# Kernel optimization log

Hardware: AMD Instinct MI355X
Metric: run time of the kernel (lower is better)

Reference implementation:

```python
import jax, jax.numpy as jnp
import numpy as np

BATCH, NUM_FEAT, EMB = 1024, 32, 16
HIDDEN = [128, 128, 128]


def setup_inputs() -> dict:
    key = jax.random.key(0)
    ks = jax.random.split(key, 4)
    inputs = jax.random.normal(ks[0], (BATCH, NUM_FEAT, EMB), dtype=jnp.float32)
    # Conv1D kernel_size=1 -> dense weight of shape (in_dim, units) per layer.
    # in_dim_i = h_{i-1} * num_feat, with h_{-1} = num_feat.
    in0 = NUM_FEAT * NUM_FEAT          # 1024
    in1 = HIDDEN[0] * NUM_FEAT         # 4096
    in2 = HIDDEN[1] * NUM_FEAT         # 4096
    scale = lambda fan_in: (1.0 / np.sqrt(fan_in)).astype(np.float32) if isinstance(fan_in, np.ndarray) else np.float32(1.0 / np.sqrt(fan_in))
    W0 = jax.random.normal(ks[1], (in0, HIDDEN[0]), dtype=jnp.float32) * scale(in0)
    W1 = jax.random.normal(ks[2], (in1, HIDDEN[1]), dtype=jnp.float32) * scale(in1)
    W2 = jax.random.normal(ks[3], (in2, HIDDEN[2]), dtype=jnp.float32) * scale(in2)
    b0 = jnp.zeros((HIDDEN[0],), dtype=jnp.float32)
    b1 = jnp.zeros((HIDDEN[1],), dtype=jnp.float32)
    b2 = jnp.zeros((HIDDEN[2],), dtype=jnp.float32)
    return {"inputs": inputs, "W0": W0, "b0": b0, "W1": W1, "b1": b1, "W2": W2, "b2": b2}


def reference(inputs, W0, b0, W1, b1, W2, b2):
    # inputs: (b, m, e) -> x0: (b, e, m)  [channels-last like tf.transpose perm=[0,2,1]]
    x0 = jnp.transpose(inputs, (0, 2, 1))
    b, d, m = x0.shape
    params = [(W0, b0), (W1, b1), (W2, b2)]
    xl = x0
    layer_outs = []
    for i, (W, bias) in enumerate(params):
        h = xl.shape[-1]
        # outer product over feature axes: (b, d, h, m) -> flatten to (b, d, h*m)
        zl = jnp.einsum('bdh,bdm->bdhm', xl, x0).reshape(b, d, h * m)
        xl = zl @ W + bias  # 1x1 conv == per-position GEMM
        if i < len(params) - 1:
            xl = jax.nn.relu(xl)
        layer_outs.append(xl)
    # sum over embedding axis d, concat over layers -> (b, sum(HIDDEN))
    return jnp.concatenate([o.sum(axis=1) for o in layer_outs], axis=1)
```

## Files before the change

### kernel.cpp

```cpp
#include <hip/hip_runtime.h>


typedef unsigned int u32;
typedef __attribute__((ext_vector_type(8))) short short8;
typedef __attribute__((ext_vector_type(4))) float f32x4;
typedef __attribute__((ext_vector_type(4))) u32 u32x4;

#define R_TOTAL 16384
#define GLOBAL_AS __attribute__((address_space(1)))
#define LDS_AS __attribute__((address_space(3)))

union PackU { u32 u[4]; short8 s; };
union PackB { u32x4 v; short8 s; };

__device__ __forceinline__ u32 pack_rne(float a, float b) {
  u32 r;
  asm("v_cvt_pk_bf16_f32 %0, %1, %2" : "=v"(r) : "v"(a), "v"(b));
  return r;
}

__device__ __forceinline__ void build_x0t_body(const float* __restrict__ in,
                                               float* __restrict__ x0t,
                                               int bid, int tid, float* t) {
  const int b0 = bid * 8;
  #pragma unroll
  for (int rep = 0; rep < 4; ++rep) {
    int idx = tid + rep * 256;
    *(float4*)&t[idx * 4] = *(const float4*)&in[(size_t)b0 * 512 + idx * 4];
  }
  __syncthreads();
  #pragma unroll
  for (int rep = 0; rep < 4; ++rep) {
    int idx = tid + rep * 256;
    int m = idx >> 5, rem = idx & 31;
    int bl = rem >> 2, dq = rem & 3;
    *(float4*)&x0t[(size_t)m * R_TOTAL + (b0 + bl) * 16 + dq * 4] =
        *(const float4*)&t[bl * 512 + m * 16 + dq * 4];
  }
}

__device__ __forceinline__ void swizzle_body(const float* __restrict__ W,
                                             u32* __restrict__ wt,
                                             int bid, int tid, float* wl) {
  const int t = bid >> 2, nq = bid & 3;
  {
    int kk = tid >> 3, c4 = tid & 7;
    float4 v = *(const float4*)&W[(size_t)(t * 32 + kk) * 128 + nq * 32 + c4 * 4];
    wl[kk * 33 + c4 * 4 + 0] = v.x;
    wl[kk * 33 + c4 * 4 + 1] = v.y;
    wl[kk * 33 + c4 * 4 + 2] = v.z;
    wl[kk * 33 + c4 * 4 + 3] = v.w;
  }
  __syncthreads();
  if (tid < 128) {
    int nl = tid >> 2, p = tid & 3;
    int q = p ^ (nl & 3);
    u32 o[4];
    #pragma unroll
    for (int jj = 0; jj < 4; ++jj)
      o[jj] = pack_rne(wl[(q * 8 + 2 * jj + 0) * 33 + nl],
                       wl[(q * 8 + 2 * jj + 1) * 33 + nl]);
    *(u32x4*)(wt + (size_t)(t * 4 + nq) * 512 + nl * 16 + p * 4) =
        u32x4{o[0], o[1], o[2], o[3]};
  }
}

__global__ __launch_bounds__(256) void prep_all(
    const float* __restrict__ in, float* __restrict__ x0t,
    const float* __restrict__ W0, u32* __restrict__ wt0,
    const float* __restrict__ W1, u32* __restrict__ wt1,
    const float* __restrict__ W2, u32* __restrict__ wt2) {
  __shared__ float sh[4096];
  const int b = blockIdx.x, tid = threadIdx.x;
  if (b < 128)      build_x0t_body(in, x0t, b, tid, sh);
  else if (b < 256) swizzle_body(W0, wt0, b - 128, tid, sh);
  else if (b < 768) swizzle_body(W1, wt1, b - 256, tid, sh);
  else              swizzle_body(W2, wt2, b - 768, tid, sh);
}

__device__ __forceinline__ void stage2k(const u32* g, u32* l, int lane) {
  const GLOBAL_AS u32* gp = (const GLOBAL_AS u32*)g;
  LDS_AS u32* lp = (LDS_AS u32*)l;
  #pragma unroll
  for (int i = 0; i < 2; ++i)
    __builtin_amdgcn_global_load_lds(gp + i * 256 + lane * 4, lp + i * 256, 16, 0, 0);
}

#define KITER(I, SLOT, WAITIMM, DO_STAGE)                                      \
  {                                                                            \
    __builtin_amdgcn_s_waitcnt(WAITIMM);                                       \
    __builtin_amdgcn_sched_barrier(0);                                         \
    f32x4 xlc[4];                                                              \
    xlc[0] = xn[SLOT][0]; xlc[1] = xn[SLOT][1];                                \
    xlc[2] = xn[SLOT][2]; xlc[3] = xn[SLOT][3];                                \
    const u32* buf = mybuf + (SLOT) * 512;                                     \
    PackB bh0, bh1;                                                            \
    {                                                                          \
      const u32* row0 = buf + ln15 * 16;                                       \
      bh0.v = *(const u32x4*)(row0 + ((q ^ sw) * 4));                          \
      const u32* row1 = buf + (16 + ln15) * 16;                                \
      bh1.v = *(const u32x4*)(row1 + ((q ^ sw) * 4));                          \
    }                                                                          \
    asm volatile("s_waitcnt lgkmcnt(0)" ::: "memory");                         \
    __builtin_amdgcn_sched_barrier(0);                                         \
    if (DO_STAGE) {                                                            \
      stage2k(wt + (size_t)((t0 + (I) + 2) * 4 + nq) * 512,                    \
              mybuf + (SLOT) * 512, lane);                                     \
      const float* xp = xt + (size_t)(t0 + (I) + 2) * R_TOTAL + r0;            \
      xn[SLOT][0] = *(const f32x4*)(xp + 0 + q * 4);                           \
      xn[SLOT][1] = *(const f32x4*)(xp + 16 + q * 4);                          \
      xn[SLOT][2] = *(const f32x4*)(xp + 32 + q * 4);                          \
      xn[SLOT][3] = *(const f32x4*)(xp + 48 + q * 4);                          \
    }                                                                          \
    __builtin_amdgcn_sched_barrier(0);                                         \
    __builtin_amdgcn_s_setprio(1);                                             \
    _Pragma("unroll")                                                          \
    for (int f = 0; f < 4; ++f) {                                              \
      f32x4 Y = __builtin_amdgcn_mfma_f32_16x16x32_bf16(Ah[f].s, bh0.s, zero4, 0, 0, 0); \
      acc[f][0] += xlc[f] * Y;                                                 \
    }                                                                          \
    _Pragma("unroll")                                                          \
    for (int f = 0; f < 4; ++f) {                                              \
      f32x4 Y = __builtin_amdgcn_mfma_f32_16x16x32_bf16(Ah[f].s, bh1.s, zero4, 0, 0, 0); \
      acc[f][1] += xlc[f] * Y;                                                 \
    }                                                                          \
    __builtin_amdgcn_s_setprio(0);                                             \
    __builtin_amdgcn_sched_barrier(0);                                         \
  }

template <int NT, bool RELU, bool STORE_X>
__global__ __launch_bounds__(512, 2) void layer_mfma(
    const float* __restrict__ xt,
    const float* __restrict__ x0t,
    const u32* __restrict__ wt,
    const float* __restrict__ bias,
    float* __restrict__ xoutT,
    float* __restrict__ osum)
{
  constexpr int HT = NT / 2;
  static_assert((HT & 1) == 0 && HT >= 4, "pair-loop needs even HT >= 4");
  __shared__ u32 smem[16384];

  const int tid = threadIdx.x;
  const int w = tid >> 6, lane = tid & 63;
  const int ln15 = lane & 15, q = lane >> 4;
  const int kh = w & 1, nq = w >> 1;
  const int r0 = blockIdx.x * 64;
  const int sw = ln15 & 3;
  u32* mybuf = smem + w * 2048;

  PackU Ah[4];
  #pragma unroll
  for (int f = 0; f < 4; ++f) {
    const int rbase = r0 + f * 16 + ln15;
    float e[8];
    #pragma unroll
    for (int j = 0; j < 8; ++j) e[j] = x0t[(size_t)(q * 8 + j) * R_TOTAL + rbase];
    #pragma unroll
    for (int jj = 0; jj < 4; ++jj)
      Ah[f].u[jj] = pack_rne(e[2 * jj], e[2 * jj + 1]);
  }

  f32x4 acc[4][2];
  #pragma unroll
  for (int f = 0; f < 4; ++f)
    #pragma unroll
    for (int c = 0; c < 2; ++c) acc[f][c] = f32x4{0.f, 0.f, 0.f, 0.f};
  const f32x4 zero4 = {0.f, 0.f, 0.f, 0.f};

  const int t0 = kh * HT;

  f32x4 xn[2][4];
  stage2k(wt + (size_t)(t0 * 4 + nq) * 512, mybuf, lane);
  {
    const float* xp = xt + (size_t)t0 * R_TOTAL + r0;
    xn[0][0] = *(const f32x4*)(xp + 0 + q * 4);
    xn[0][1] = *(const f32x4*)(xp + 16 + q * 4);
    xn[0][2] = *(const f32x4*)(xp + 32 + q * 4);
    xn[0][3] = *(const f32x4*)(xp + 48 + q * 4);
  }
  stage2k(wt + (size_t)((t0 + 1) * 4 + nq) * 512, mybuf + 512, lane);
  {
    const float* xp = xt + (size_t)(t0 + 1) * R_TOTAL + r0;
    xn[1][0] = *(const f32x4*)(xp + 0 + q * 4);
    xn[1][1] = *(const f32x4*)(xp + 16 + q * 4);
    xn[1][2] = *(const f32x4*)(xp + 32 + q * 4);
    xn[1][3] = *(const f32x4*)(xp + 48 + q * 4);
  }
  __builtin_amdgcn_sched_barrier(0);

  for (int i = 0; i < HT - 2; i += 2) {
    KITER(i, 0, 0x0F76, 1);
    KITER(i + 1, 1, 0x0F76, 1);
  }
  KITER(HT - 2, 0, 0x0F76, 0);
  KITER(HT - 1, 1, 0x0F70, 0);

  __syncthreads();
  if (kh == 1) {
    u32* reg = mybuf;
    #pragma unroll
    for (int f = 0; f < 4; ++f)
      #pragma unroll
      for (int c = 0; c < 2; ++c)
        *(f32x4*)(reg + ((size_t)(f * 2 + c) * 64 + lane) * 4) = acc[f][c];
  }
  __syncthreads();
  if (kh == 0) {
    const u32* reg = smem + (w + 1) * 2048;
    float bs[2];
    #pragma unroll
    for (int c = 0; c < 2; ++c) bs[c] = bias[nq * 32 + c * 16 + ln15];

    f32x4 vv[4][2];
    #pragma unroll
    for (int f = 0; f < 4; ++f) {
      #pragma unroll
      for (int c = 0; c < 2; ++c) {
        f32x4 part = *(const f32x4*)(reg + ((size_t)(f * 2 + c) * 64 + lane) * 4);
        f32x4 v = acc[f][c] + part;
        v.x += bs[c]; v.y += bs[c]; v.z += bs[c]; v.w += bs[c];
        if (RELU) {
          v.x = fmaxf(v.x, 0.f); v.y = fmaxf(v.y, 0.f);
          v.z = fmaxf(v.z, 0.f); v.w = fmaxf(v.w, 0.f);
        }
        vv[f][c] = v;
        float s = v.x + v.y + v.z + v.w;
        s += __shfl_xor(s, 16, 64);
        s += __shfl_xor(s, 32, 64);
        if (q == 0)
          osum[(size_t)((r0 >> 4) + f) * 384 + nq * 32 + c * 16 + ln15] = s;
      }
    }

    if (STORE_X) {
      u32* myreg = mybuf;
      #pragma unroll
      for (int f = 0; f < 4; ++f)
        #pragma unroll
        for (int c = 0; c < 2; ++c)
          *(f32x4*)(myreg + ((size_t)(f * 2 + c) * 64 + lane) * 4) = vv[f][c];
      #pragma unroll
      for (int c = 0; c < 2; ++c) {
        #pragma unroll
        for (int s = 0; s < 4; ++s) {
          f32x4 vr = *(const f32x4*)(myreg +
              ((size_t)(s * 2 + c) * 64 + (lane & 3) * 16 + (lane >> 2)) * 4);
          const int col = nq * 32 + c * 16 + (lane >> 2);
          *(f32x4*)&xoutT[(size_t)col * R_TOTAL + r0 + s * 16 + (lane & 3) * 4] = vr;
        }
      }
    }
  }
}

extern "C" void kernel_launch(void* const* d_in, const int* in_sizes, int n_in,
                              void* d_out, int out_size, void* d_ws, size_t ws_size,
                              hipStream_t stream) {
  const float* in = (const float*)d_in[0];
  const float* W0 = (const float*)d_in[1];
  const float* b0 = (const float*)d_in[2];
  const float* W1 = (const float*)d_in[3];
  const float* b1 = (const float*)d_in[4];
  const float* W2 = (const float*)d_in[5];
  const float* b2 = (const float*)d_in[6];
  float* out = (float*)d_out;

  float* X0T = (float*)d_ws;
  float* X1T = X0T + (size_t)32 * R_TOTAL;
  float* X2T = X1T + (size_t)128 * R_TOTAL;
  u32* Wt0 = (u32*)(X2T + (size_t)128 * R_TOTAL);
  u32* Wt1 = Wt0 + (size_t)32 * 4 * 512;
  u32* Wt2 = Wt1 + (size_t)128 * 4 * 512;

  prep_all<<<1280, 256, 0, stream>>>(in, X0T, W0, Wt0, W1, Wt1, W2, Wt2);

  layer_mfma<32, true, true><<<256, 512, 0, stream>>>(X0T, X0T, Wt0, b0, X1T, out + 0);
  layer_mfma<128, true, true><<<256, 512, 0, stream>>>(X1T, X0T, Wt1, b1, X2T, out + 128);
  layer_mfma<128, false, false><<<256, 512, 0, stream>>>(X2T, X0T, Wt2, b2, nullptr, out + 256);
}
```

Baseline: 137.7 us.

## Software-pipeline LDS B-fragment reads one iteration ahead of MFMAs

Each k-iteration now reads the next slot's B fragments from LDS before issuing the current slot's MFMAs, using double-buffered register fragments and retuned vmcnt/lgkmcnt wait immediates. The MFMAs are grouped ahead of the scale-accumulate, and the xn global reloads are moved after the compute. This aims to hide LDS read latency and the lgkmcnt(0) stall behind MFMA work. It adds register pressure and depends on hand-encoded waitcnt values being correct for the reordered loads.

```diff
diff --git a/kernel.cpp b/kernel.cpp
--- a/kernel.cpp
+++ b/kernel.cpp
@@ -86,46 +86,48 @@
     __builtin_amdgcn_global_load_lds(gp + i * 256 + lane * 4, lp + i * 256, 16, 0, 0);
 }
 
-#define KITER(I, SLOT, WAITIMM, DO_STAGE)                                      \
+#define SB() __builtin_amdgcn_sched_barrier(0)
+
+#define KITER(I, SLOT, TOPVM, LGKM, DO_STAGE, READ_NEXT, BCUR, BNXT)           \
   {                                                                            \
-    __builtin_amdgcn_s_waitcnt(WAITIMM);                                       \
-    __builtin_amdgcn_sched_barrier(0);                                         \
-    f32x4 xlc[4];                                                              \
-    xlc[0] = xn[SLOT][0]; xlc[1] = xn[SLOT][1];                                \
-    xlc[2] = xn[SLOT][2]; xlc[3] = xn[SLOT][3];                                \
-    const u32* buf = mybuf + (SLOT) * 512;                                     \
-    PackB bh0, bh1;                                                            \
-    {                                                                          \
-      const u32* row0 = buf + ln15 * 16;                                       \
-      bh0.v = *(const u32x4*)(row0 + ((q ^ sw) * 4));                          \
-      const u32* row1 = buf + (16 + ln15) * 16;                                \
-      bh1.v = *(const u32x4*)(row1 + ((q ^ sw) * 4));                          \
-    }                                                                          \
-    asm volatile("s_waitcnt lgkmcnt(0)" ::: "memory");                         \
-    __builtin_amdgcn_sched_barrier(0);                                         \
+    __builtin_amdgcn_s_waitcnt(TOPVM);                                         \
+    SB();                                                                      \
+    if (READ_NEXT) {                                                           \
+      const u32* nbuf = mybuf + ((SLOT) ^ 1) * 512;                            \
+      BNXT[0].v = *(const u32x4*)(nbuf + ln15 * 16 + ((q ^ sw) * 4));          \
+      BNXT[1].v = *(const u32x4*)(nbuf + (16 + ln15) * 16 + ((q ^ sw) * 4));   \
+    }                                                                          \
+    SB();                                                                      \
+    __builtin_amdgcn_s_waitcnt(LGKM);                                          \
+    SB();                                                                      \
     if (DO_STAGE) {                                                            \
       stage2k(wt + (size_t)((t0 + (I) + 2) * 4 + nq) * 512,                    \
               mybuf + (SLOT) * 512, lane);                                     \
+    }                                                                          \
+    SB();                                                                      \
+    __builtin_amdgcn_s_setprio(1);                                             \
+    f32x4 Y0[4], Y1[4];                                                        \
+    _Pragma("unroll")                                                          \
+    for (int f = 0; f < 4; ++f)                                                \
+      Y0[f] = __builtin_amdgcn_mfma_f32_16x16x32_bf16(Ah[f].s, BCUR[0].s, zero4, 0, 0, 0); \
+    _Pragma("unroll")                                                          \
+    for (int f = 0; f < 4; ++f)                                                \
+      Y1[f] = __builtin_amdgcn_mfma_f32_16x16x32_bf16(Ah[f].s, BCUR[1].s, zero4, 0, 0, 0); \
+    _Pragma("unroll")                                                          \
+    for (int f = 0; f < 4; ++f) {                                              \
+      acc[f][0] += xn[SLOT][f] * Y0[f];                                        \
+      acc[f][1] += xn[SLOT][f] * Y1[f];                                        \
+    }                                                                          \
+    __builtin_amdgcn_s_setprio(0);                                             \
+    SB();                                                                      \
+    if (DO_STAGE) {                                                            \
       const float* xp = xt + (size_t)(t0 + (I) + 2) * R_TOTAL + r0;            \
       xn[SLOT][0] = *(const f32x4*)(xp + 0 + q * 4);                           \
       xn[SLOT][1] = *(const f32x4*)(xp + 16 + q * 4);                          \
       xn[SLOT][2] = *(const f32x4*)(xp + 32 + q * 4);                          \
       xn[SLOT][3] = *(const f32x4*)(xp + 48 + q * 4);                          \
     }                                                                          \
-    __builtin_amdgcn_sched_barrier(0);                                         \
-    __builtin_amdgcn_s_setprio(1);                                             \
-    _Pragma("unroll")                                                          \
-    for (int f = 0; f < 4; ++f) {                                              \
-      f32x4 Y = __builtin_amdgcn_mfma_f32_16x16x32_bf16(Ah[f].s, bh0.s, zero4, 0, 0, 0); \
-      acc[f][0] += xlc[f] * Y;                                                 \
-    }                                                                          \
-    _Pragma("unroll")                                                          \
-    for (int f = 0; f < 4; ++f) {                                              \
-      f32x4 Y = __builtin_amdgcn_mfma_f32_16x16x32_bf16(Ah[f].s, bh1.s, zero4, 0, 0, 0); \
-      acc[f][1] += xlc[f] * Y;                                                 \
-    }                                                                          \
-    __builtin_amdgcn_s_setprio(0);                                             \
-    __builtin_amdgcn_sched_barrier(0);                                         \
+    SB();                                                                      \
   }
 
 template <int NT, bool RELU, bool STORE_X>
@@ -172,6 +174,7 @@
 
   f32x4 xn[2][4];
   stage2k(wt + (size_t)(t0 * 4 + nq) * 512, mybuf, lane);
+  SB();
   {
     const float* xp = xt + (size_t)t0 * R_TOTAL + r0;
     xn[0][0] = *(const f32x4*)(xp + 0 + q * 4);
@@ -179,7 +182,9 @@
     xn[0][2] = *(const f32x4*)(xp + 32 + q * 4);
     xn[0][3] = *(const f32x4*)(xp + 48 + q * 4);
   }
+  SB();
   stage2k(wt + (size_t)((t0 + 1) * 4 + nq) * 512, mybuf + 512, lane);
+  SB();
   {
     const float* xp = xt + (size_t)(t0 + 1) * R_TOTAL + r0;
     xn[1][0] = *(const f32x4*)(xp + 0 + q * 4);
@@ -187,14 +192,22 @@
     xn[1][2] = *(const f32x4*)(xp + 32 + q * 4);
     xn[1][3] = *(const f32x4*)(xp + 48 + q * 4);
   }
-  __builtin_amdgcn_sched_barrier(0);
+  SB();
+  __builtin_amdgcn_s_waitcnt(0x0F7A);
+  SB();
+  PackB ba[2], bb[2];
+  {
+    ba[0].v = *(const u32x4*)(mybuf + ln15 * 16 + ((q ^ sw) * 4));
+    ba[1].v = *(const u32x4*)(mybuf + (16 + ln15) * 16 + ((q ^ sw) * 4));
+  }
+  SB();
 
   for (int i = 0; i < HT - 2; i += 2) {
-    KITER(i, 0, 0x0F76, 1);
-    KITER(i + 1, 1, 0x0F76, 1);
-  }
-  KITER(HT - 2, 0, 0x0F76, 0);
-  KITER(HT - 1, 1, 0x0F70, 0);
+    KITER(i,     0, 0x0F74, 0xC27F, 1, 1, ba, bb);
+    KITER(i + 1, 1, 0x0F74, 0xC27F, 1, 1, bb, ba);
+  }
+  KITER(HT - 2, 0, 0x0F74, 0xC27F, 0, 1, ba, bb);
+  KITER(HT - 1, 1, 0x0F70, 0xC07F, 0, 0, bb, ba);
 
   __syncthreads();
   if (kh == 1) {
```

Result: no change. 137.2 us (-0.4%).
